# Kernel tuning notes

Measured on AMD Instinct MI355X. Metric: run time of the kernel, lower is better.

The kernel has to match this reference:

```python
import jax, jax.numpy as jnp
import numpy as np

NUM_USERS = 100000
NUM_ITEMS = 50000
HIDDEN = [256, 128, 64]
BATCH = 1024


def setup_inputs() -> dict:
    key = jax.random.key(0)
    ks = jax.random.split(key, 12)
    user_ids = jax.random.randint(ks[0], (BATCH,), 0, NUM_USERS, dtype=jnp.int32)
    item_ids = jax.random.randint(ks[1], (BATCH,), 0, NUM_ITEMS, dtype=jnp.int32)
    in_dim = NUM_USERS + NUM_ITEMS
    # Linear weights stored [in, out] for x @ W + b
    W1 = jax.random.normal(ks[2], (in_dim, HIDDEN[0]), dtype=jnp.float32) * 0.01
    b1 = jnp.zeros((HIDDEN[0],), dtype=jnp.float32)
    W2 = jax.random.normal(ks[3], (HIDDEN[0], HIDDEN[1]), dtype=jnp.float32) * 0.05
    b2 = jnp.zeros((HIDDEN[1],), dtype=jnp.float32)
    W3 = jax.random.normal(ks[4], (HIDDEN[1], HIDDEN[2]), dtype=jnp.float32) * 0.05
    b3 = jnp.zeros((HIDDEN[2],), dtype=jnp.float32)
    W4 = jax.random.normal(ks[5], (HIDDEN[2], 1), dtype=jnp.float32) * 0.05
    b4 = jnp.zeros((1,), dtype=jnp.float32)
    return {"user_ids": user_ids, "item_ids": item_ids,
            "W1": W1, "b1": b1, "W2": W2, "b2": b2,
            "W3": W3, "b3": b3, "W4": W4, "b4": b4}


def reference(user_ids, item_ids, W1, b1, W2, b2, W3, b3, W4, b4):
    # one_hot(user) @ W1[:NUM_USERS] + one_hot(item) @ W1[NUM_USERS:] == row gathers
    h = W1[user_ids] + W1[NUM_USERS + item_ids] + b1  # [B, 256]
    h = jax.nn.relu(h)
    h = jax.nn.relu(h @ W2 + b2)                       # [B, 128]
    h = jax.nn.relu(h @ W3 + b3)                       # [B, 64]
    return h @ W4 + b4                                 # [B, 1]
```

## Files before the change

kernel.cpp:

```cpp
#include <hip/hip_runtime.h>

#define NUM_USERS 100000
#define H1 256
#define H2 128
#define H3 64
#define BATCH 1024

__global__ __launch_bounds__(256) void mlp_row(
    const int* __restrict__ user_ids,
    const int* __restrict__ item_ids,
    const float* __restrict__ W1, const float* __restrict__ b1,
    const float* __restrict__ W2, const float* __restrict__ b2,
    const float* __restrict__ W3, const float* __restrict__ b3,
    const float* __restrict__ W4, const float* __restrict__ b4,
    float* __restrict__ out)
{
    __shared__ float h1[H1];
    __shared__ float h2[H2];
    __shared__ float h3[H3];
    __shared__ float res;

    const int t   = threadIdx.x;
    const int row = blockIdx.x;

    const int u  = user_ids[row];
    const int it = item_ids[row];

    {
        float v = W1[(size_t)u * H1 + t]
                + W1[(size_t)(NUM_USERS + it) * H1 + t]
                + b1[t];
        h1[t] = v > 0.f ? v : 0.f;
    }
    __syncthreads();

    if (t < H2) {
        float acc = b2[t];
        for (int k = 0; k < H1; ++k)
            acc += h1[k] * W2[k * H2 + t];
        h2[t] = acc > 0.f ? acc : 0.f;
    }
    __syncthreads();

    if (t < H3) {
        float acc = b3[t];
        for (int k = 0; k < H2; ++k)
            acc += h2[k] * W3[k * H3 + t];
        h3[t] = acc > 0.f ? acc : 0.f;
    }
    __syncthreads();

    if (t == 0) {
        float acc = b4[0];
        for (int k = 0; k < H3; ++k)
            acc += h3[k] * W4[k];
        res = acc;
    }
    __syncthreads();

    if (t < 64)
        out[row] = res;
}

extern "C" void kernel_launch(void* const* d_in, const int* in_sizes, int n_in,
                              void* d_out, int out_size, void* d_ws, size_t ws_size,
                              hipStream_t stream) {
    const int*   user_ids = (const int*)d_in[0];
    const int*   item_ids = (const int*)d_in[1];
    const float* W1 = (const float*)d_in[2];
    const float* b1 = (const float*)d_in[3];
    const float* W2 = (const float*)d_in[4];
    const float* b2 = (const float*)d_in[5];
    const float* W3 = (const float*)d_in[6];
    const float* b3 = (const float*)d_in[7];
    const float* W4 = (const float*)d_in[8];
    const float* b4 = (const float*)d_in[9];
    float* out = (float*)d_out;

    dim3 grid(BATCH);
    dim3 block(256);
    mlp_row<<<grid, block, 0, stream>>>(user_ids, item_ids,
                                        W1, b1, W2, b2, W3, b3, W4, b4, out);
}
```

Baseline: 210.9 us.

## Split hidden-layer dot products across all threads and reduce final layer with shuffles

Layers 2 and 3 now use all 256 threads: each thread computes a partial dot product over a K-slice, with float4 LDS reads and four independent FMA accumulators, and the partials are summed through shared memory. The final 64-wide dot product moves from a serial single-thread loop to a wavefront shuffle reduction, which also removes two barriers. The aim is to cut the serial dependency chains and idle threads in the per-row MLP, at the cost of extra shared memory and an additional partial-sum pass.

```diff
diff --git a/kernel.cpp b/kernel.cpp
--- a/kernel.cpp
+++ b/kernel.cpp
@@ -15,10 +15,10 @@
     const float* __restrict__ W4, const float* __restrict__ b4,
     float* __restrict__ out)
 {
-    __shared__ float h1[H1];
-    __shared__ float h2[H2];
-    __shared__ float h3[H3];
-    __shared__ float res;
+    __shared__ __align__(16) float h1[H1];
+    __shared__ __align__(16) float p2[256];
+    __shared__ __align__(16) float h2[H2];
+    __shared__ __align__(16) float p3[256];
 
     const int t   = threadIdx.x;
     const int row = blockIdx.x;
@@ -34,32 +34,60 @@
     }
     __syncthreads();
 
+    {
+        const int j  = t & (H2 - 1);
+        const int k0 = (t >> 7) << 7;
+        const float4* h1v = (const float4*)(h1 + k0);
+        const float* __restrict__ w2c = W2 + j;
+        float a0 = 0.f, a1 = 0.f, a2 = 0.f, a3 = 0.f;
+        #pragma unroll
+        for (int k4 = 0; k4 < 32; ++k4) {
+            const float4 h = h1v[k4];
+            const int kk = k0 + (k4 << 2);
+            a0 = fmaf(h.x, w2c[(size_t)(kk    ) * H2], a0);
+            a1 = fmaf(h.y, w2c[(size_t)(kk + 1) * H2], a1);
+            a2 = fmaf(h.z, w2c[(size_t)(kk + 2) * H2], a2);
+            a3 = fmaf(h.w, w2c[(size_t)(kk + 3) * H2], a3);
+        }
+        p2[t] = (a0 + a1) + (a2 + a3);
+    }
+    __syncthreads();
     if (t < H2) {
-        float acc = b2[t];
-        for (int k = 0; k < H1; ++k)
-            acc += h1[k] * W2[k * H2 + t];
-        h2[t] = acc > 0.f ? acc : 0.f;
+        const float s = p2[t] + p2[t + 128] + b2[t];
+        h2[t] = s > 0.f ? s : 0.f;
+    }
+    __syncthreads();
+
+    {
+        const int j  = t & (H3 - 1);
+        const int k0 = (t >> 6) << 5;
+        const float4* h2v = (const float4*)(h2 + k0);
+        const float* __restrict__ w3c = W3 + j;
+        float a0 = 0.f, a1 = 0.f, a2 = 0.f, a3 = 0.f;
+        #pragma unroll
+        for (int k4 = 0; k4 < 8; ++k4) {
+            const float4 h = h2v[k4];
+            const int kk = k0 + (k4 << 2);
+            a0 = fmaf(h.x, w3c[(size_t)(kk    ) * H3], a0);
+            a1 = fmaf(h.y, w3c[(size_t)(kk + 1) * H3], a1);
+            a2 = fmaf(h.z, w3c[(size_t)(kk + 2) * H3], a2);
+            a3 = fmaf(h.w, w3c[(size_t)(kk + 3) * H3], a3);
+        }
+        p3[t] = (a0 + a1) + (a2 + a3);
     }
     __syncthreads();
 
     if (t < H3) {
-        float acc = b3[t];
-        for (int k = 0; k < H2; ++k)
-            acc += h2[k] * W3[k * H3 + t];
-        h3[t] = acc > 0.f ? acc : 0.f;
+        const float s = ((p3[t] + p3[t + 64]) + (p3[t + 128] + p3[t + 192]))
+                      + b3[t];
+        const float h3v = s > 0.f ? s : 0.f;
+        float pv = h3v * W4[t];
+        #pragma unroll
+        for (int off = 32; off > 0; off >>= 1)
+            pv += __shfl_down(pv, off, 64);
+        if (t == 0)
+            out[row] = pv + b4[0];
     }
-    __syncthreads();
-
-    if (t == 0) {
-        float acc = b4[0];
-        for (int k = 0; k < H3; ++k)
-            acc += h3[k] * W4[k];
-        res = acc;
-    }
-    __syncthreads();
-
-    if (t < 64)
-        out[row] = res;
 }
 
 extern "C" void kernel_launch(void* const* d_in, const int* in_sizes, int n_in,
```

After: 204.8 us. -2.9%, faster.

## Map one wavefront per batch row and replace shared memory with lane broadcasts

Applied to the files above, without the earlier changes.

Each 64-lane wavefront now handles one batch row, so each block covers four rows and the grid shrinks by four. Hidden activations stay in registers and are broadcast with readlane instead of going through shared memory, which removes all __syncthreads. The final dot product becomes a shuffle reduction. Loads use float4 for the W1 rows and float2 for W2, and split accumulators add ILP. The aim is to stop the many idle threads in the later layers, which wasted most of each block in the old code.

```diff
diff --git a/kernel.cpp b/kernel.cpp
--- a/kernel.cpp
+++ b/kernel.cpp
@@ -5,6 +5,10 @@
 #define H2 128
 #define H3 64
 #define BATCH 1024
+
+__device__ __forceinline__ float lane_bcast(float v, int lane) {
+    return __uint_as_float(__builtin_amdgcn_readlane(__float_as_uint(v), lane));
+}
 
 __global__ __launch_bounds__(256) void mlp_row(
     const int* __restrict__ user_ids,
@@ -15,51 +19,72 @@
     const float* __restrict__ W4, const float* __restrict__ b4,
     float* __restrict__ out)
 {
-    __shared__ float h1[H1];
-    __shared__ float h2[H2];
-    __shared__ float h3[H3];
-    __shared__ float res;
-
-    const int t   = threadIdx.x;
-    const int row = blockIdx.x;
+    const int t    = threadIdx.x;
+    const int wave = t >> 6;
+    const int lane = t & 63;
+    const int row  = blockIdx.x * 4 + wave;
 
     const int u  = user_ids[row];
     const int it = item_ids[row];
 
+    float hk[4];
     {
-        float v = W1[(size_t)u * H1 + t]
-                + W1[(size_t)(NUM_USERS + it) * H1 + t]
-                + b1[t];
-        h1[t] = v > 0.f ? v : 0.f;
+        const float4 wu = ((const float4*)(W1 + (size_t)u * H1))[lane];
+        const float4 wi = ((const float4*)(W1 + (size_t)(NUM_USERS + it) * H1))[lane];
+        const float4 bb = ((const float4*)b1)[lane];
+        const float v0 = wu.x + wi.x + bb.x;
+        const float v1 = wu.y + wi.y + bb.y;
+        const float v2 = wu.z + wi.z + bb.z;
+        const float v3 = wu.w + wi.w + bb.w;
+        hk[0] = v0 > 0.f ? v0 : 0.f;
+        hk[1] = v1 > 0.f ? v1 : 0.f;
+        hk[2] = v2 > 0.f ? v2 : 0.f;
+        hk[3] = v3 > 0.f ? v3 : 0.f;
     }
-    __syncthreads();
 
-    if (t < H2) {
-        float acc = b2[t];
-        for (int k = 0; k < H1; ++k)
-            acc += h1[k] * W2[k * H2 + t];
-        h2[t] = acc > 0.f ? acc : 0.f;
+    float2 acc[4] = {{0.f,0.f},{0.f,0.f},{0.f,0.f},{0.f,0.f}};
+    {
+        const float2* __restrict__ W2v = (const float2*)W2;
+        #pragma unroll
+        for (int k = 0; k < H1; ++k) {
+            const float  hs = lane_bcast(hk[k & 3], k >> 2);
+            const float2 w  = W2v[(size_t)k * (H2 / 2) + lane];
+            acc[k & 3].x = fmaf(hs, w.x, acc[k & 3].x);
+            acc[k & 3].y = fmaf(hs, w.y, acc[k & 3].y);
+        }
     }
-    __syncthreads();
+    float h2a, h2b;
+    {
+        const float2 bv = ((const float2*)b2)[lane];
+        const float sa = ((acc[0].x + acc[1].x) + (acc[2].x + acc[3].x)) + bv.x;
+        const float sb = ((acc[0].y + acc[1].y) + (acc[2].y + acc[3].y)) + bv.y;
+        h2a = sa > 0.f ? sa : 0.f;
+        h2b = sb > 0.f ? sb : 0.f;
+    }
 
-    if (t < H3) {
-        float acc = b3[t];
-        for (int k = 0; k < H2; ++k)
-            acc += h2[k] * W3[k * H3 + t];
-        h3[t] = acc > 0.f ? acc : 0.f;
+    float c0 = 0.f, c1 = 0.f, c2 = 0.f, c3 = 0.f;
+    {
+        #pragma unroll
+        for (int k = 0; k < H2; k += 4) {
+            const float s0 = lane_bcast(h2a, (k    ) >> 1);
+            const float s1 = lane_bcast(h2b, (k + 1) >> 1);
+            const float s2 = lane_bcast(h2a, (k + 2) >> 1);
+            const float s3 = lane_bcast(h2b, (k + 3) >> 1);
+            c0 = fmaf(s0, W3[(size_t)(k    ) * H3 + lane], c0);
+            c1 = fmaf(s1, W3[(size_t)(k + 1) * H3 + lane], c1);
+            c2 = fmaf(s2, W3[(size_t)(k + 2) * H3 + lane], c2);
+            c3 = fmaf(s3, W3[(size_t)(k + 3) * H3 + lane], c3);
+        }
     }
-    __syncthreads();
+    const float s3s = ((c0 + c1) + (c2 + c3)) + b3[lane];
+    const float h3v = s3s > 0.f ? s3s : 0.f;
 
-    if (t == 0) {
-        float acc = b4[0];
-        for (int k = 0; k < H3; ++k)
-            acc += h3[k] * W4[k];
-        res = acc;
-    }
-    __syncthreads();
-
-    if (t < 64)
-        out[row] = res;
+    float pv = h3v * W4[lane];
+    #pragma unroll
+    for (int off = 32; off > 0; off >>= 1)
+        pv += __shfl_xor(pv, off, 64);
+    if (lane == 0)
+        out[row] = pv + b4[0];
 }
 
 extern "C" void kernel_launch(void* const* d_in, const int* in_sizes, int n_in,
@@ -77,7 +102,7 @@
     const float* b4 = (const float*)d_in[9];
     float* out = (float*)d_out;
 
-    dim3 grid(BATCH);
+    dim3 grid(BATCH / 4);
     dim3 block(256);
     mlp_row<<<grid, block, 0, stream>>>(user_ids, item_ids,
                                         W1, b1, W2, b2, W3, b3, W4, b4, out);
```

New measurement: 208.0 us. Within noise of the previous version (-1.4%).

## Process four batch rows per block with split-K and wave-shuffle reduction

Applied to the files above, without the earlier changes.

Each block now handles four batch rows, so every W2/W3 weight load is reused across four rows held as transposed float4 vectors in shared memory. All 256 threads work in layers 2 and 3 by splitting the K dimension, with partial sums combined through shared memory. The final 64-wide dot product uses wave shuffles instead of a single-thread serial loop. This cuts redundant weight traffic and idle threads, but launches only 256 blocks, which lowers parallelism across the GPU.

```diff
diff --git a/kernel.cpp b/kernel.cpp
--- a/kernel.cpp
+++ b/kernel.cpp
@@ -6,7 +6,7 @@
 #define H3 64
 #define BATCH 1024
 
-__global__ __launch_bounds__(256) void mlp_row(
+__global__ __launch_bounds__(256) void mlp_row4(
     const int* __restrict__ user_ids,
     const int* __restrict__ item_ids,
     const float* __restrict__ W1, const float* __restrict__ b1,
@@ -15,51 +15,129 @@
     const float* __restrict__ W4, const float* __restrict__ b4,
     float* __restrict__ out)
 {
-    __shared__ float h1[H1];
-    __shared__ float h2[H2];
-    __shared__ float h3[H3];
-    __shared__ float res;
+    __shared__ __align__(16) float h1T[H1][4];
+    __shared__ __align__(16) float p2[H2][4];
+    __shared__ __align__(16) float h2T[H2][4];
+    __shared__ __align__(16) float p3[3][H3][4];
 
-    const int t   = threadIdx.x;
-    const int row = blockIdx.x;
-
-    const int u  = user_ids[row];
-    const int it = item_ids[row];
+    const int t    = threadIdx.x;
+    const int wave = t >> 6;
+    const int lane = t & 63;
+    const int row0 = blockIdx.x << 2;
 
     {
-        float v = W1[(size_t)u * H1 + t]
-                + W1[(size_t)(NUM_USERS + it) * H1 + t]
-                + b1[t];
-        h1[t] = v > 0.f ? v : 0.f;
+        const int u  = user_ids[row0 + wave];
+        const int it = item_ids[row0 + wave];
+        const float* __restrict__ ru = W1 + (size_t)u * H1;
+        const float* __restrict__ ri = W1 + (size_t)(NUM_USERS + it) * H1;
+        #pragma unroll
+        for (int i = 0; i < 4; ++i) {
+            const int k = lane + (i << 6);
+            const float v = ru[k] + ri[k] + b1[k];
+            h1T[k][wave] = v > 0.f ? v : 0.f;
+        }
     }
     __syncthreads();
 
-    if (t < H2) {
-        float acc = b2[t];
-        for (int k = 0; k < H1; ++k)
-            acc += h1[k] * W2[k * H2 + t];
-        h2[t] = acc > 0.f ? acc : 0.f;
+    const int j2 = t & (H2 - 1);
+    const int kh = t >> 7;
+    float a[4][2] = {};
+    {
+        const float* __restrict__ w2c = W2 + j2;
+        const int kbase = kh << 7;
+        #pragma unroll
+        for (int kk = 0; kk < 128; kk += 2) {
+            const float4 hA = *(const float4*)&h1T[kbase + kk    ][0];
+            const float4 hB = *(const float4*)&h1T[kbase + kk + 1][0];
+            const float wA = w2c[(size_t)(kbase + kk    ) * H2];
+            const float wB = w2c[(size_t)(kbase + kk + 1) * H2];
+            a[0][0] = fmaf(hA.x, wA, a[0][0]);  a[0][1] = fmaf(hB.x, wB, a[0][1]);
+            a[1][0] = fmaf(hA.y, wA, a[1][0]);  a[1][1] = fmaf(hB.y, wB, a[1][1]);
+            a[2][0] = fmaf(hA.z, wA, a[2][0]);  a[2][1] = fmaf(hB.z, wB, a[2][1]);
+            a[3][0] = fmaf(hA.w, wA, a[3][0]);  a[3][1] = fmaf(hB.w, wB, a[3][1]);
+        }
+    }
+    if (kh == 1) {
+        float4 pp;
+        pp.x = a[0][0] + a[0][1];
+        pp.y = a[1][0] + a[1][1];
+        pp.z = a[2][0] + a[2][1];
+        pp.w = a[3][0] + a[3][1];
+        *(float4*)&p2[j2][0] = pp;
+    }
+    __syncthreads();
+    if (kh == 0) {
+        const float bb = b2[j2];
+        float4 hh;
+        {
+            const float s0 = (a[0][0] + a[0][1]) + p2[j2][0] + bb;
+            const float s1 = (a[1][0] + a[1][1]) + p2[j2][1] + bb;
+            const float s2 = (a[2][0] + a[2][1]) + p2[j2][2] + bb;
+            const float s3 = (a[3][0] + a[3][1]) + p2[j2][3] + bb;
+            hh.x = s0 > 0.f ? s0 : 0.f;
+            hh.y = s1 > 0.f ? s1 : 0.f;
+            hh.z = s2 > 0.f ? s2 : 0.f;
+            hh.w = s3 > 0.f ? s3 : 0.f;
+        }
+        *(float4*)&h2T[j2][0] = hh;
+    }
+    __syncthreads();
+
+    const int j3 = t & (H3 - 1);
+    const int kq = t >> 6;
+    float c[4][2] = {};
+    {
+        const float* __restrict__ w3c = W3 + j3;
+        const int kbase = kq << 5;
+        #pragma unroll
+        for (int kk = 0; kk < 32; kk += 2) {
+            const float4 hA = *(const float4*)&h2T[kbase + kk    ][0];
+            const float4 hB = *(const float4*)&h2T[kbase + kk + 1][0];
+            const float wA = w3c[(size_t)(kbase + kk    ) * H3];
+            const float wB = w3c[(size_t)(kbase + kk + 1) * H3];
+            c[0][0] = fmaf(hA.x, wA, c[0][0]);  c[0][1] = fmaf(hB.x, wB, c[0][1]);
+            c[1][0] = fmaf(hA.y, wA, c[1][0]);  c[1][1] = fmaf(hB.y, wB, c[1][1]);
+            c[2][0] = fmaf(hA.z, wA, c[2][0]);  c[2][1] = fmaf(hB.z, wB, c[2][1]);
+            c[3][0] = fmaf(hA.w, wA, c[3][0]);  c[3][1] = fmaf(hB.w, wB, c[3][1]);
+        }
+    }
+    if (kq != 0) {
+        float4 pp;
+        pp.x = c[0][0] + c[0][1];
+        pp.y = c[1][0] + c[1][1];
+        pp.z = c[2][0] + c[2][1];
+        pp.w = c[3][0] + c[3][1];
+        *(float4*)&p3[kq - 1][j3][0] = pp;
     }
     __syncthreads();
 
     if (t < H3) {
-        float acc = b3[t];
-        for (int k = 0; k < H2; ++k)
-            acc += h2[k] * W3[k * H3 + t];
-        h3[t] = acc > 0.f ? acc : 0.f;
+        const float bb = b3[t];
+        float h3r[4];
+        #pragma unroll
+        for (int r = 0; r < 4; ++r) {
+            const float s = ((c[r][0] + c[r][1]) + p3[0][t][r])
+                          + (p3[1][t][r] + p3[2][t][r]) + bb;
+            h3r[r] = s > 0.f ? s : 0.f;
+        }
+        const float w4 = W4[t];
+        float pv0 = h3r[0] * w4, pv1 = h3r[1] * w4;
+        float pv2 = h3r[2] * w4, pv3 = h3r[3] * w4;
+        #pragma unroll
+        for (int off = 32; off > 0; off >>= 1) {
+            pv0 += __shfl_xor(pv0, off, 64);
+            pv1 += __shfl_xor(pv1, off, 64);
+            pv2 += __shfl_xor(pv2, off, 64);
+            pv3 += __shfl_xor(pv3, off, 64);
+        }
+        if (t == 0) {
+            const float bo = b4[0];
+            float4 o;
+            o.x = pv0 + bo;  o.y = pv1 + bo;
+            o.z = pv2 + bo;  o.w = pv3 + bo;
+            *(float4*)(out + row0) = o;
+        }
     }
-    __syncthreads();
-
-    if (t == 0) {
-        float acc = b4[0];
-        for (int k = 0; k < H3; ++k)
-            acc += h3[k] * W4[k];
-        res = acc;
-    }
-    __syncthreads();
-
-    if (t < 64)
-        out[row] = res;
 }
 
 extern "C" void kernel_launch(void* const* d_in, const int* in_sizes, int n_in,
@@ -77,8 +155,8 @@
     const float* b4 = (const float*)d_in[9];
     float* out = (float*)d_out;
 
-    dim3 grid(BATCH);
+    dim3 grid(BATCH / 4);
     dim3 block(256);
-    mlp_row<<<grid, block, 0, stream>>>(user_ids, item_ids,
-                                        W1, b1, W2, b2, W3, b3, W4, b4, out);
+    mlp_row4<<<grid, block, 0, stream>>>(user_ids, item_ids,
+                                         W1, b1, W2, b2, W3, b3, W4, b4, out);
 }
```

Result: no change. 207.1 us (-1.8%).
